# Kernel optimization log

Hardware: AMD Instinct MI355X
Metric: run time of the kernel (lower is better)

## Reference

```python
import jax, jax.numpy as jnp
import numpy as np

B = 4          # batch_size (config.batch_size)
N = 17000      # num_prots (nodes per graph)
F_IN = 256     # num_features
C = 128        # out_channels
E = 2176000    # num edges (avg degree 32)
NODES = B * N


def _gcn_layer(x, W, b, src, dst, n):
    """PyG GCNConv: add self-loops, sym-normalized aggregation, then bias.
    out[i] = sum_{j->i} d_j^{-1/2} d_i^{-1/2} (x_j W) + d_i^{-1} (x_i W) + b
    with d = degree(dst) + 1 (self loop)."""
    h = x @ W  # [n, C]
    deg = jax.ops.segment_sum(jnp.ones(src.shape[0], x.dtype), dst, num_segments=n) + 1.0
    dinv = jax.lax.rsqrt(deg)  # [n]
    coef = dinv[src] * dinv[dst]                      # [E]
    agg = jax.ops.segment_sum(h[src] * coef[:, None], dst, num_segments=n)
    agg = agg + h * (dinv * dinv)[:, None]            # self-loop term
    return agg + b


def setup_inputs() -> dict:
    key = jax.random.key(0)
    ks = jax.random.split(key, 16)

    def glorot(k, shape):
        fan_in, fan_out = shape[0], shape[1]
        s = jnp.sqrt(6.0 / (fan_in + fan_out))
        return jax.random.uniform(k, shape, jnp.float32, -s, s)

    inp = {
        "x": jax.random.normal(ks[0], (NODES, F_IN), jnp.float32),
        "edge_index": jax.random.randint(ks[1], (2, E), 0, NODES, jnp.int32),
        "protein_mask": jax.random.randint(ks[2], (B, N), 0, 2, jnp.int32),
        "W1": glorot(ks[3], (F_IN, C)), "b1": jnp.zeros((C,), jnp.float32),
        "W2": glorot(ks[4], (C, C)),    "b2": jnp.zeros((C,), jnp.float32),
        "W3": glorot(ks[5], (C, C)),    "b3": jnp.zeros((C,), jnp.float32),
        "lw1": glorot(ks[6], (C, 256)), "lb1": jnp.zeros((256,), jnp.float32),
        "lw2": glorot(ks[7], (256, 64)), "lb2": jnp.zeros((64,), jnp.float32),
        "lw3": glorot(ks[8], (64, 16)),  "lb3": jnp.zeros((16,), jnp.float32),
        "lw4": glorot(ks[9], (16, 1)),   "lb4": jnp.zeros((1,), jnp.float32),
    }
    return inp


def reference(x, edge_index, protein_mask, W1, b1, W2, b2, W3, b3,
              lw1, lb1, lw2, lb2, lw3, lb3, lw4, lb4):
    src, dst = edge_index[0], edge_index[1]
    h1 = jax.nn.relu(_gcn_layer(x, W1, b1, src, dst, NODES))   # [NODES, C]
    h2 = jax.nn.relu(_gcn_layer(h1, W2, b2, src, dst, NODES))
    h3 = jax.nn.relu(_gcn_layer(h2, W3, b3, src, dst, NODES))
    s = (h1 + h2 + h3).reshape(B, N, C)                        # residual sum
    mask = protein_mask.astype(jnp.float32)                    # [B, N]
    pooled = jnp.einsum('bn,bnc->bc', mask, s)                 # masked bmm pool [B, C]
    z = jax.nn.relu(pooled @ lw1 + lb1)
    z = jax.nn.relu(z @ lw2 + lb2)
    z = jax.nn.relu(z @ lw3 + lb3)
    return z @ lw4 + lb4                                       # [B, 1]
```

## Files before the change

### kernel.cpp

```cpp
#include <hip/hip_runtime.h>
#include <hip/hip_bf16.h>
#include <cstdint>

#define F_IN 256
#define C 128
#define NBUK_MAX 320
#define CHUNK 4096

typedef short bf8_t __attribute__((ext_vector_type(8)));
typedef float f4_t  __attribute__((ext_vector_type(4)));

static inline size_t align256(size_t x) { return (x + 255) & ~(size_t)255; }


__global__ __launch_bounds__(256) void histA_kernel(const int* __restrict__ dst,
                                                    int* __restrict__ btot,
                                                    int E, int nbuk) {
    __shared__ int hist[NBUK_MAX];
    const int tid = threadIdx.x;
    const int e0 = blockIdx.x * CHUNK;
    for (int i = tid; i < NBUK_MAX; i += 256) hist[i] = 0;
    __syncthreads();
#pragma unroll
    for (int k = 0; k < CHUNK / 256; ++k) {
        int e = e0 + k * 256 + tid;
        if (e < E) atomicAdd(&hist[dst[e] >> 8], 1);
    }
    __syncthreads();
    for (int i = tid; i < nbuk; i += 256) {
        int h = hist[i];
        if (h) atomicAdd(&btot[i], h);
    }
}

__global__ __launch_bounds__(256) void bscan_kernel(const int* __restrict__ btot,
                                                    int nbuk,
                                                    int* __restrict__ ebase,
                                                    int* __restrict__ gcur) {
    __shared__ int sums[NBUK_MAX];
    __shared__ int base[NBUK_MAX + 1];
    const int tid = threadIdx.x;
    for (int bk = tid; bk < NBUK_MAX; bk += 256)
        sums[bk] = (bk < nbuk) ? btot[bk] : 0;
    __syncthreads();
    if (tid < 64) {
        int acc[5];
        int s = 0;
#pragma unroll
        for (int j = 0; j < 5; ++j) {
            acc[j] = s;
            s += sums[tid * 5 + j];
        }
        int tot = s;
#pragma unroll
        for (int d = 1; d < 64; d <<= 1) {
            int o = __shfl_up(tot, d);
            if (tid >= d) tot += o;
        }
        int excl = tot - s;
#pragma unroll
        for (int j = 0; j < 5; ++j) base[tid * 5 + j] = excl + acc[j];
        if (tid == 63) base[320] = tot;
    }
    __syncthreads();
    for (int bk = tid; bk <= nbuk; bk += 256) {
        ebase[bk] = base[bk];
        if (bk < nbuk) gcur[bk] = base[bk];
    }
}

__global__ __launch_bounds__(256) void partition_kernel(const int* __restrict__ src,
                                                        const int* __restrict__ dst,
                                                        int* __restrict__ gcur,
                                                        int2* __restrict__ ebuf, int E) {
    __shared__ int hist[NBUK_MAX];
    __shared__ int base[NBUK_MAX];
    __shared__ int gbase[NBUK_MAX];
    __shared__ int2 stage[CHUNK];
    const int tid = threadIdx.x;
    const int e0 = blockIdx.x * CHUNK;
    const int cnt = min(CHUNK, E - e0);

    for (int i = tid; i < NBUK_MAX; i += 256) hist[i] = 0;
    __syncthreads();

    int2 ev[CHUNK / 256];
    int mo[CHUNK / 256];
#pragma unroll
    for (int k = 0; k < CHUNK / 256; ++k) {
        int e = e0 + k * 256 + tid;
        if (e < E) {
            int2 v;
            v.x = src[e];
            v.y = dst[e];
            ev[k] = v;
            mo[k] = atomicAdd(&hist[v.y >> 8], 1);
        }
    }
    __syncthreads();
    if (tid < 64) {
        int acc[5];
        int s = 0;
#pragma unroll
        for (int j = 0; j < 5; ++j) {
            int idx = tid * 5 + j;
            acc[j] = s;
            s += hist[idx];
        }
        int tot = s;
#pragma unroll
        for (int d = 1; d < 64; d <<= 1) {
            int o = __shfl_up(tot, d);
            if (tid >= d) tot += o;
        }
        int excl = tot - s;
#pragma unroll
        for (int j = 0; j < 5; ++j) base[tid * 5 + j] = excl + acc[j];
    }
    __syncthreads();
    for (int i = tid; i < NBUK_MAX; i += 256) {
        int h = hist[i];
        gbase[i] = h ? atomicAdd(&gcur[i], h) : 0;
    }
    __syncthreads();
#pragma unroll
    for (int k = 0; k < CHUNK / 256; ++k) {
        int e = e0 + k * 256 + tid;
        if (e < E) stage[base[ev[k].y >> 8] + mo[k]] = ev[k];
    }
    __syncthreads();
    for (int i = tid; i < cnt; i += 256) {
        int2 e = stage[i];
        int b = e.y >> 8;
        ebuf[gbase[b] + (i - base[b])] = e;
    }
}

__global__ __launch_bounds__(256) void csr_build_kernel(const int2* __restrict__ ebuf,
                                                        const int* __restrict__ ebase,
                                                        int* __restrict__ offs,
                                                        float* __restrict__ dinv,
                                                        int* __restrict__ csr, int nodes) {
    __shared__ int deg[256];
    __shared__ int p[256];
    __shared__ int pre[257];
    __shared__ int cur[256];
    const int b = blockIdx.x;
    const int n0 = b << 8;
    const int ncnt = min(256, nodes - n0);
    const int tid = threadIdx.x;
    const int eb = ebase[b], ee = ebase[b + 1];

    deg[tid] = 0;
    __syncthreads();
    for (int i = eb + tid; i < ee; i += 256)
        atomicAdd(&deg[ebuf[i].y & 255], 1);
    __syncthreads();
    p[tid] = deg[tid];
    __syncthreads();
    for (int d = 1; d < 256; d <<= 1) {
        int v = (tid >= d) ? p[tid - d] : 0;
        __syncthreads();
        p[tid] += v;
        __syncthreads();
    }
    pre[tid + 1] = p[tid];
    if (tid == 0) pre[0] = 0;
    __syncthreads();

    for (int i = tid; i <= ncnt; i += 256)
        offs[n0 + i] = eb + pre[i] + n0 + i;
    if (tid < ncnt) {
        dinv[n0 + tid] = rsqrtf((float)(deg[tid] + 1));
        csr[eb + pre[tid] + n0 + tid] = n0 + tid;
    }
    cur[tid] = 0;
    __syncthreads();
    for (int i = eb + tid; i < ee; i += 256) {
        int2 e = ebuf[i];
        int loc = e.y & 255;
        int q = atomicAdd(&cur[loc], 1);
        csr[eb + pre[loc] + n0 + loc + 1 + q] = e.x;
    }
}

static __device__ inline unsigned pack_bf16(float a, float b) {
    __hip_bfloat162 h = __float22bfloat162_rn(make_float2(a, b));
    return *(unsigned*)&h;
}

__global__ void wswz_kernel(const float* __restrict__ W, __hip_bfloat16* __restrict__ Wsw,
                            int K) {
    int i = blockIdx.x * blockDim.x + threadIdx.x;
    int total = (K >> 5) * 8 * 64;
    if (i < total) {
        int l = i & 63;
        int u = (i >> 6) & 7;
        int t = i >> 9;
        int krow = t * 32 + (l >> 4) * 8;
        int col = u * 16 + (l & 15);
        unsigned packed[4];
#pragma unroll
        for (int j = 0; j < 4; ++j) {
            float a = W[(size_t)(krow + 2 * j) * C + col];
            float b = W[(size_t)(krow + 2 * j + 1) * C + col];
            packed[j] = pack_bf16(a, b);
        }
        uint4 o = make_uint4(packed[0], packed[1], packed[2], packed[3]);
        *(uint4*)(Wsw + (size_t)i * 8) = o;
    }
}


static __device__ inline bf8_t pack8(float4 u0, float4 u1) {
    union { unsigned u[4]; bf8_t v; } r;
    r.u[0] = pack_bf16(u0.x, u0.y);
    r.u[1] = pack_bf16(u0.z, u0.w);
    r.u[2] = pack_bf16(u1.x, u1.y);
    r.u[3] = pack_bf16(u1.z, u1.w);
    return r.v;
}

template <bool F32IN>
__global__ __launch_bounds__(256) void mfma_gemm_kernel(const void* __restrict__ Xv,
                                                        const __hip_bfloat16* __restrict__ Wsw,
                                                        const float* __restrict__ dinv,
                                                        __hip_bfloat16* __restrict__ G,
                                                        int M, int K) {
    extern __shared__ char lds[];
    const int tid = threadIdx.x;
    const int l = tid & 63;
    const int w = tid >> 6;
    const int lm = l & 15;
    const int lk = (l >> 4) * 8;
    const int row0 = blockIdx.x * 128 + w * 32;

    const int bytes = K * 256;
    for (int o = tid * 16; o < bytes; o += 256 * 16)
        *(uint4*)(lds + o) = *(const uint4*)((const char*)Wsw + o);
    __syncthreads();

    f4_t acc[2][8] = {};
    const int steps = K >> 5;
    const int r0 = min(row0 + lm, M - 1);
    const int r1 = min(row0 + 16 + lm, M - 1);

    const float* xf0 = (const float*)Xv + (size_t)r0 * K + lk;
    const float* xf1 = (const float*)Xv + (size_t)r1 * K + lk;
    const __hip_bfloat16* xb0 = (const __hip_bfloat16*)Xv + (size_t)r0 * K + lk;
    const __hip_bfloat16* xb1 = (const __hip_bfloat16*)Xv + (size_t)r1 * K + lk;

    for (int t = 0; t < steps; ++t) {
        bf8_t a0, a1;
        if (F32IN) {
            float4 u0 = *(const float4*)(xf0 + t * 32);
            float4 u1 = *(const float4*)(xf0 + t * 32 + 4);
            float4 v0 = *(const float4*)(xf1 + t * 32);
            float4 v1 = *(const float4*)(xf1 + t * 32 + 4);
            a0 = pack8(u0, u1);
            a1 = pack8(v0, v1);
        } else {
            a0 = *(const bf8_t*)(xb0 + t * 32);
            a1 = *(const bf8_t*)(xb1 + t * 32);
        }
        const char* bbase = lds + ((size_t)(t * 8) * 64 + l) * 16;
#pragma unroll
        for (int u = 0; u < 8; ++u) {
            bf8_t b = *(const bf8_t*)(bbase + (size_t)u * 64 * 16);
            acc[0][u] = __builtin_amdgcn_mfma_f32_16x16x32_bf16(a0, b, acc[0][u], 0, 0, 0);
            acc[1][u] = __builtin_amdgcn_mfma_f32_16x16x32_bf16(a1, b, acc[1][u], 0, 0, 0);
        }
    }

#pragma unroll
    for (int mt = 0; mt < 2; ++mt) {
        int rbase = row0 + mt * 16 + (l >> 4) * 4;
#pragma unroll
        for (int r = 0; r < 4; ++r) {
            int row = rbase + r;
            if (row < M) {
                float dv = dinv[row];
#pragma unroll
                for (int u = 0; u < 8; ++u) {
                    float v = acc[mt][u][r] * dv;
                    G[(size_t)row * C + u * 16 + lm] = __float2bfloat16(v);
                }
            }
        }
    }
}

__global__ __launch_bounds__(64) void agg_kernel(const __hip_bfloat16* __restrict__ G,
                                                 const int* __restrict__ csr,
                                                 const int* __restrict__ offs,
                                                 const float* __restrict__ dinv,
                                                 const float* __restrict__ bias,
                                                 __hip_bfloat16* __restrict__ A) {
    __shared__ int s_i[64];
    const int node = blockIdx.x;
    const int tid = threadIdx.x;
    const int c0 = tid * 2;
    const int beg = offs[node], end = offs[node + 1];
    float accx = 0.f, accy = 0.f;
    for (int base = beg; base < end; base += 64) {
        int cnt = min(64, end - base);
        if (tid < cnt) s_i[tid] = csr[base + tid];
        __syncthreads();
#pragma unroll 4
        for (int j = 0; j < cnt; ++j) {
            __hip_bfloat162 hv = *(const __hip_bfloat162*)(G + (size_t)s_i[j] * C + c0);
            float2 f = __bfloat1622float2(hv);
            accx += f.x;
            accy += f.y;
        }
        __syncthreads();
    }
    float d = dinv[node];
    float ox = fmaxf(accx * d + bias[c0], 0.f);
    float oy = fmaxf(accy * d + bias[c0 + 1], 0.f);
    __hip_bfloat162 o = __float22bfloat162_rn(make_float2(ox, oy));
    *(__hip_bfloat162*)(A + (size_t)node * C + c0) = o;
}

__global__ __launch_bounds__(64) void pool_kernel(const __hip_bfloat16* __restrict__ S,
                                                  const int* __restrict__ mask,
                                                  float* __restrict__ pooled, int N) {
    const int b = blockIdx.y;
    const int n0 = blockIdx.x * 128;
    const int c0 = threadIdx.x * 2;
    const int lim = min(n0 + 128, N);
    float ax = 0.f, ay = 0.f;
    for (int n = n0; n < lim; ++n) {
        if (mask[b * N + n]) {
            __hip_bfloat162 hv = *(const __hip_bfloat162*)(S + ((size_t)b * N + n) * C + c0);
            float2 f = __bfloat1622float2(hv);
            ax += f.x;
            ay += f.y;
        }
    }
    atomicAdd(&pooled[b * C + c0], ax);
    atomicAdd(&pooled[b * C + c0 + 1], ay);
}

__global__ __launch_bounds__(256) void mlp_kernel(const float* __restrict__ pooled,
        const float* __restrict__ lw1, const float* __restrict__ lb1,
        const float* __restrict__ lw2, const float* __restrict__ lb2,
        const float* __restrict__ lw3, const float* __restrict__ lb3,
        const float* __restrict__ lw4, const float* __restrict__ lb4,
        float* __restrict__ out) {
    __shared__ float p[4 * 128];
    __shared__ float z1[4 * 256];
    __shared__ float z2[4 * 64];
    __shared__ float z3[4 * 16];
    const int tid = threadIdx.x;
    for (int i = tid; i < 4 * 128; i += 256) p[i] = pooled[i];
    __syncthreads();
    for (int o = tid; o < 4 * 256; o += 256) {
        int b = o >> 8, j = o & 255;
        float s = lb1[j];
        for (int k = 0; k < 128; ++k) s += p[b * 128 + k] * lw1[k * 256 + j];
        z1[o] = fmaxf(s, 0.f);
    }
    __syncthreads();
    for (int o = tid; o < 4 * 64; o += 256) {
        int b = o >> 6, j = o & 63;
        float s = lb2[j];
        for (int k = 0; k < 256; ++k) s += z1[b * 256 + k] * lw2[k * 64 + j];
        z2[o] = fmaxf(s, 0.f);
    }
    __syncthreads();
    if (tid < 64) {
        int b = tid >> 4, j = tid & 15;
        float s = lb3[j];
        for (int k = 0; k < 64; ++k) s += z2[b * 64 + k] * lw3[k * 16 + j];
        z3[tid] = fmaxf(s, 0.f);
    }
    __syncthreads();
    if (tid < 4) {
        float s = lb4[0];
        for (int k = 0; k < 16; ++k) s += z3[tid * 16 + k] * lw4[k];
        out[tid] = s;
    }
}


extern "C" void kernel_launch(void* const* d_in, const int* in_sizes, int n_in,
                              void* d_out, int out_size, void* d_ws, size_t ws_size,
                              hipStream_t stream) {
    const float* x    = (const float*)d_in[0];
    const int*   ei   = (const int*)d_in[1];
    const int*   pmask = (const int*)d_in[2];
    const float* W1 = (const float*)d_in[3];  const float* b1 = (const float*)d_in[4];
    const float* W2 = (const float*)d_in[5];  const float* b2 = (const float*)d_in[6];
    const float* W3 = (const float*)d_in[7];  const float* b3 = (const float*)d_in[8];
    const float* lw1 = (const float*)d_in[9];  const float* lb1 = (const float*)d_in[10];
    const float* lw2 = (const float*)d_in[11]; const float* lb2 = (const float*)d_in[12];
    const float* lw3 = (const float*)d_in[13]; const float* lb3 = (const float*)d_in[14];
    const float* lw4 = (const float*)d_in[15]; const float* lb4 = (const float*)d_in[16];
    float* out = (float*)d_out;

    const int E = in_sizes[1] / 2;
    const int NODES = in_sizes[0] / F_IN;
    const int NB = 4;
    const int NPER = NODES / NB;
    const int NBUK = (NODES + 255) >> 8;
    const int NBLK = (E + CHUNK - 1) / CHUNK;
    const int* esrc = ei;
    const int* edst = ei + E;

    char* w = (char*)d_ws;
    size_t off = 0;
    auto alloc = [&](size_t bytes) -> void* {
        void* p = w + off;
        off = align256(off + bytes);
        return p;
    };
    float* dinv = (float*)alloc((size_t)NODES * 4);
    int*   offs = (int*)  alloc((size_t)(NODES + 1) * 4);
    int*   ebase = (int*) alloc((size_t)(NBUK + 1) * 4);
    int*   gcur = (int*)  alloc((size_t)NBUK * 4);
    int*   btot = (int*)  alloc((size_t)NBUK * 4);
    int2*  ebuf = (int2*) alloc((size_t)E * 8);
    int*   csr  = (int*)  alloc((size_t)(E + NODES) * 4);
    __hip_bfloat16* G   = (__hip_bfloat16*)alloc((size_t)NODES * C * 2);
    __hip_bfloat16* A1  = (__hip_bfloat16*)alloc((size_t)NODES * C * 2);
    __hip_bfloat16* A2  = (__hip_bfloat16*)alloc((size_t)NODES * C * 2);
    __hip_bfloat16* Wsw = (__hip_bfloat16*)alloc((size_t)F_IN * C * 2);
    float* pooled = (float*)alloc((size_t)4 * C * 4);
    (void)ws_size; (void)n_in; (void)out_size;

    hipMemsetAsync(pooled, 0, (size_t)4 * C * 4, stream);
    hipMemsetAsync(btot,   0, (size_t)NBUK * 4, stream);

    histA_kernel<<<NBLK, 256, 0, stream>>>(edst, btot, E, NBUK);
    bscan_kernel<<<1, 256, 0, stream>>>(btot, NBUK, ebase, gcur);
    partition_kernel<<<NBLK, 256, 0, stream>>>(esrc, edst, gcur, ebuf, E);
    csr_build_kernel<<<NBUK, 256, 0, stream>>>(ebuf, ebase, offs, dinv, csr, NODES);

    const int gblocks = (NODES + 127) / 128;
    dim3 pgrid((NPER + 127) / 128, NB);

    wswz_kernel<<<(F_IN / 32 * 512 + 255) / 256, 256, 0, stream>>>(W1, Wsw, F_IN);
    mfma_gemm_kernel<true><<<gblocks, 256, F_IN * 256, stream>>>(x, Wsw, dinv, G, NODES, F_IN);
    agg_kernel<<<NODES, 64, 0, stream>>>(G, csr, offs, dinv, b1, A1);
    pool_kernel<<<pgrid, 64, 0, stream>>>(A1, pmask, pooled, NPER);
    wswz_kernel<<<(C / 32 * 512 + 255) / 256, 256, 0, stream>>>(W2, Wsw, C);
    mfma_gemm_kernel<false><<<gblocks, 256, C * 256, stream>>>(A1, Wsw, dinv, G, NODES, C);
    agg_kernel<<<NODES, 64, 0, stream>>>(G, csr, offs, dinv, b2, A2);
    pool_kernel<<<pgrid, 64, 0, stream>>>(A2, pmask, pooled, NPER);
    wswz_kernel<<<(C / 32 * 512 + 255) / 256, 256, 0, stream>>>(W3, Wsw, C);
    mfma_gemm_kernel<false><<<gblocks, 256, C * 256, stream>>>(A2, Wsw, dinv, G, NODES, C);
    agg_kernel<<<NODES, 64, 0, stream>>>(G, csr, offs, dinv, b3, A1);
    pool_kernel<<<pgrid, 64, 0, stream>>>(A1, pmask, pooled, NPER);

    mlp_kernel<<<1, 256, 0, stream>>>(pooled, lw1, lb1, lw2, lb2, lw3, lb3, lw4, lb4, out);
}
```

Measured before the change: 579.3 us.

## Prefetch GEMM A-tiles, template rows per wave, shuffle-broadcast agg indices

The MFMA GEMM now takes a compile-time row-tile count per wave and software-prefetches the next K-step of X into registers while the current step's MFMAs run. The 128-wide layers use 4 row tiles per wave, so each block covers 256 rows. The aggregation kernel drops its LDS index staging and two barriers per chunk, broadcasting neighbor indices with wave shuffles and unrolling the gather by 8. All weight swizzles are hoisted to the start into separate buffers, which costs more registers in the GEMM and extra workspace.

```diff
diff --git a/kernel.cpp b/kernel.cpp
--- a/kernel.cpp
+++ b/kernel.cpp
@@ -221,7 +221,7 @@
     return r.v;
 }
 
-template <bool F32IN>
+template <bool F32IN, int MT>
 __global__ __launch_bounds__(256) void mfma_gemm_kernel(const void* __restrict__ Xv,
                                                         const __hip_bfloat16* __restrict__ Wsw,
                                                         const float* __restrict__ dinv,
@@ -233,47 +233,77 @@
     const int w = tid >> 6;
     const int lm = l & 15;
     const int lk = (l >> 4) * 8;
-    const int row0 = blockIdx.x * 128 + w * 32;
+    const int row0 = blockIdx.x * (MT * 64) + w * (MT * 16);
 
     const int bytes = K * 256;
     for (int o = tid * 16; o < bytes; o += 256 * 16)
         *(uint4*)(lds + o) = *(const uint4*)((const char*)Wsw + o);
     __syncthreads();
 
-    f4_t acc[2][8] = {};
+    f4_t acc[MT][8] = {};
     const int steps = K >> 5;
-    const int r0 = min(row0 + lm, M - 1);
-    const int r1 = min(row0 + 16 + lm, M - 1);
-
-    const float* xf0 = (const float*)Xv + (size_t)r0 * K + lk;
-    const float* xf1 = (const float*)Xv + (size_t)r1 * K + lk;
-    const __hip_bfloat16* xb0 = (const __hip_bfloat16*)Xv + (size_t)r0 * K + lk;
-    const __hip_bfloat16* xb1 = (const __hip_bfloat16*)Xv + (size_t)r1 * K + lk;
+
+    const float* xf[MT];
+    const __hip_bfloat16* xb[MT];
+#pragma unroll
+    for (int mt = 0; mt < MT; ++mt) {
+        int r = min(row0 + mt * 16 + lm, M - 1);
+        xf[mt] = (const float*)Xv + (size_t)r * K + lk;
+        xb[mt] = (const __hip_bfloat16*)Xv + (size_t)r * K + lk;
+    }
+
+    float4 cf[MT][2];
+    bf8_t cb[MT];
+#pragma unroll
+    for (int mt = 0; mt < MT; ++mt) {
+        if (F32IN) {
+            cf[mt][0] = *(const float4*)(xf[mt]);
+            cf[mt][1] = *(const float4*)(xf[mt] + 4);
+        } else {
+            cb[mt] = *(const bf8_t*)(xb[mt]);
+        }
+    }
 
     for (int t = 0; t < steps; ++t) {
-        bf8_t a0, a1;
-        if (F32IN) {
-            float4 u0 = *(const float4*)(xf0 + t * 32);
-            float4 u1 = *(const float4*)(xf0 + t * 32 + 4);
-            float4 v0 = *(const float4*)(xf1 + t * 32);
-            float4 v1 = *(const float4*)(xf1 + t * 32 + 4);
-            a0 = pack8(u0, u1);
-            a1 = pack8(v0, v1);
-        } else {
-            a0 = *(const bf8_t*)(xb0 + t * 32);
-            a1 = *(const bf8_t*)(xb1 + t * 32);
-        }
+        float4 nf[MT][2];
+        bf8_t nb[MT];
+        if (t + 1 < steps) {
+#pragma unroll
+            for (int mt = 0; mt < MT; ++mt) {
+                if (F32IN) {
+                    nf[mt][0] = *(const float4*)(xf[mt] + (t + 1) * 32);
+                    nf[mt][1] = *(const float4*)(xf[mt] + (t + 1) * 32 + 4);
+                } else {
+                    nb[mt] = *(const bf8_t*)(xb[mt] + (t + 1) * 32);
+                }
+            }
+        }
+        bf8_t a[MT];
+#pragma unroll
+        for (int mt = 0; mt < MT; ++mt)
+            a[mt] = F32IN ? pack8(cf[mt][0], cf[mt][1]) : cb[mt];
+
         const char* bbase = lds + ((size_t)(t * 8) * 64 + l) * 16;
 #pragma unroll
         for (int u = 0; u < 8; ++u) {
             bf8_t b = *(const bf8_t*)(bbase + (size_t)u * 64 * 16);
-            acc[0][u] = __builtin_amdgcn_mfma_f32_16x16x32_bf16(a0, b, acc[0][u], 0, 0, 0);
-            acc[1][u] = __builtin_amdgcn_mfma_f32_16x16x32_bf16(a1, b, acc[1][u], 0, 0, 0);
-        }
-    }
-
-#pragma unroll
-    for (int mt = 0; mt < 2; ++mt) {
+#pragma unroll
+            for (int mt = 0; mt < MT; ++mt)
+                acc[mt][u] = __builtin_amdgcn_mfma_f32_16x16x32_bf16(a[mt], b, acc[mt][u], 0, 0, 0);
+        }
+#pragma unroll
+        for (int mt = 0; mt < MT; ++mt) {
+            if (F32IN) {
+                cf[mt][0] = nf[mt][0];
+                cf[mt][1] = nf[mt][1];
+            } else {
+                cb[mt] = nb[mt];
+            }
+        }
+    }
+
+#pragma unroll
+    for (int mt = 0; mt < MT; ++mt) {
         int rbase = row0 + mt * 16 + (l >> 4) * 4;
 #pragma unroll
         for (int r = 0; r < 4; ++r) {
@@ -296,28 +326,36 @@
                                                  const float* __restrict__ dinv,
                                                  const float* __restrict__ bias,
                                                  __hip_bfloat16* __restrict__ A) {
-    __shared__ int s_i[64];
     const int node = blockIdx.x;
     const int tid = threadIdx.x;
     const int c0 = tid * 2;
     const int beg = offs[node], end = offs[node + 1];
-    float accx = 0.f, accy = 0.f;
+    float ax = 0.f, ay = 0.f;
     for (int base = beg; base < end; base += 64) {
-        int cnt = min(64, end - base);
-        if (tid < cnt) s_i[tid] = csr[base + tid];
-        __syncthreads();
-#pragma unroll 4
-        for (int j = 0; j < cnt; ++j) {
-            __hip_bfloat162 hv = *(const __hip_bfloat162*)(G + (size_t)s_i[j] * C + c0);
+        const int cnt = min(64, end - base);
+        int myidx = (tid < cnt) ? csr[base + tid] : 0;
+        int j = 0;
+        for (; j + 8 <= cnt; j += 8) {
+#pragma unroll
+            for (int u = 0; u < 8; ++u) {
+                int idx = __shfl(myidx, j + u);
+                __hip_bfloat162 hv = *(const __hip_bfloat162*)(G + (size_t)idx * C + c0);
+                float2 f = __bfloat1622float2(hv);
+                ax += f.x;
+                ay += f.y;
+            }
+        }
+        for (; j < cnt; ++j) {
+            int idx = __shfl(myidx, j);
+            __hip_bfloat162 hv = *(const __hip_bfloat162*)(G + (size_t)idx * C + c0);
             float2 f = __bfloat1622float2(hv);
-            accx += f.x;
-            accy += f.y;
-        }
-        __syncthreads();
+            ax += f.x;
+            ay += f.y;
+        }
     }
     float d = dinv[node];
-    float ox = fmaxf(accx * d + bias[c0], 0.f);
-    float oy = fmaxf(accy * d + bias[c0 + 1], 0.f);
+    float ox = fmaxf(ax * d + bias[c0], 0.f);
+    float oy = fmaxf(ay * d + bias[c0 + 1], 0.f);
     __hip_bfloat162 o = __float22bfloat162_rn(make_float2(ox, oy));
     *(__hip_bfloat162*)(A + (size_t)node * C + c0) = o;
 }
@@ -425,31 +463,35 @@
     __hip_bfloat16* G   = (__hip_bfloat16*)alloc((size_t)NODES * C * 2);
     __hip_bfloat16* A1  = (__hip_bfloat16*)alloc((size_t)NODES * C * 2);
     __hip_bfloat16* A2  = (__hip_bfloat16*)alloc((size_t)NODES * C * 2);
-    __hip_bfloat16* Wsw = (__hip_bfloat16*)alloc((size_t)F_IN * C * 2);
+    __hip_bfloat16* Wsw1 = (__hip_bfloat16*)alloc((size_t)F_IN * C * 2);
+    __hip_bfloat16* Wsw2 = (__hip_bfloat16*)alloc((size_t)C * C * 2);
+    __hip_bfloat16* Wsw3 = (__hip_bfloat16*)alloc((size_t)C * C * 2);
     float* pooled = (float*)alloc((size_t)4 * C * 4);
     (void)ws_size; (void)n_in; (void)out_size;
 
     hipMemsetAsync(pooled, 0, (size_t)4 * C * 4, stream);
     hipMemsetAsync(btot,   0, (size_t)NBUK * 4, stream);
+
+    wswz_kernel<<<(F_IN / 32 * 512 + 255) / 256, 256, 0, stream>>>(W1, Wsw1, F_IN);
+    wswz_kernel<<<(C / 32 * 512 + 255) / 256, 256, 0, stream>>>(W2, Wsw2, C);
+    wswz_kernel<<<(C / 32 * 512 + 255) / 256, 256, 0, stream>>>(W3, Wsw3, C);
 
     histA_kernel<<<NBLK, 256, 0, stream>>>(edst, btot, E, NBUK);
     bscan_kernel<<<1, 256, 0, stream>>>(btot, NBUK, ebase, gcur);
     partition_kernel<<<NBLK, 256, 0, stream>>>(esrc, edst, gcur, ebuf, E);
     csr_build_kernel<<<NBUK, 256, 0, stream>>>(ebuf, ebase, offs, dinv, csr, NODES);
 
-    const int gblocks = (NODES + 127) / 128;
+    const int gblocks128 = (NODES + 127) / 128;
+    const int gblocks256 = (NODES + 255) / 256;
     dim3 pgrid((NPER + 127) / 128, NB);
 
-    wswz_kernel<<<(F_IN / 32 * 512 + 255) / 256, 256, 0, stream>>>(W1, Wsw, F_IN);
-    mfma_gemm_kernel<true><<<gblocks, 256, F_IN * 256, stream>>>(x, Wsw, dinv, G, NODES, F_IN);
+    mfma_gemm_kernel<true, 2><<<gblocks128, 256, F_IN * 256, stream>>>(x, Wsw1, dinv, G, NODES, F_IN);
     agg_kernel<<<NODES, 64, 0, stream>>>(G, csr, offs, dinv, b1, A1);
     pool_kernel<<<pgrid, 64, 0, stream>>>(A1, pmask, pooled, NPER);
-    wswz_kernel<<<(C / 32 * 512 + 255) / 256, 256, 0, stream>>>(W2, Wsw, C);
-    mfma_gemm_kernel<false><<<gblocks, 256, C * 256, stream>>>(A1, Wsw, dinv, G, NODES, C);
+    mfma_gemm_kernel<false, 4><<<gblocks256, 256, C * 256, stream>>>(A1, Wsw2, dinv, G, NODES, C);
     agg_kernel<<<NODES, 64, 0, stream>>>(G, csr, offs, dinv, b2, A2);
     pool_kernel<<<pgrid, 64, 0, stream>>>(A2, pmask, pooled, NPER);
-    wswz_kernel<<<(C / 32 * 512 + 255) / 256, 256, 0, stream>>>(W3, Wsw, C);
-    mfma_gemm_kernel<false><<<gblocks, 256, C * 256, stream>>>(A2, Wsw, dinv, G, NODES, C);
+    mfma_gemm_kernel<false, 4><<<gblocks256, 256, C * 256, stream>>>(A2, Wsw3, dinv, G, NODES, C);
     agg_kernel<<<NODES, 64, 0, stream>>>(G, csr, offs, dinv, b3, A1);
     pool_kernel<<<pgrid, 64, 0, stream>>>(A1, pmask, pooled, NPER);
 
```

Result: no change. 590.5 us (+1.9%).
